# Kernel tuning notes

Hardware: AMD Instinct MI355X
Metric: run time of the kernel (lower is better)

Reference implementation:

```python
import jax, jax.numpy as jnp
import numpy as np

B, S, HID = 2, 2048, 2048
HQ, HKV, D = 32, 4, 128
EPS = 1e-6
SCALE = D ** -0.5


def _rms_norm(x, w):
    # per-head RMSNorm over last dim, computed in fp32 like the torch module
    xf = x.astype(jnp.float32)
    var = jnp.mean(xf * xf, axis=-1, keepdims=True)
    return (w * (xf * jax.lax.rsqrt(var + EPS))).astype(x.dtype)


def _rotate_half(x):
    x1, x2 = jnp.split(x, 2, axis=-1)
    return jnp.concatenate([-x2, x1], axis=-1)


def setup_inputs() -> dict:
    key = jax.random.key(0)
    ks = jax.random.split(key, 8)
    hidden_states = jax.random.normal(ks[0], (B, S, HID), dtype=jnp.float32)
    # RoPE tables (HF Qwen style, theta=1e6)
    inv_freq = 1.0 / (1e6 ** (np.arange(0, D, 2, dtype=np.float32) / D))
    t = np.arange(S, dtype=np.float32)
    freqs = np.outer(t, inv_freq)                      # [S, D/2]
    emb = np.concatenate([freqs, freqs], axis=-1)      # [S, D]
    cos = jnp.asarray(np.cos(emb))
    sin = jnp.asarray(np.sin(emb))
    sd = HID ** -0.5
    wq = jax.random.normal(ks[1], (HID, HQ * D), dtype=jnp.float32) * sd
    wk = jax.random.normal(ks[2], (HID, HKV * D), dtype=jnp.float32) * sd
    wv = jax.random.normal(ks[3], (HID, HKV * D), dtype=jnp.float32) * sd
    wo = jax.random.normal(ks[4], (HQ * D, HID), dtype=jnp.float32) * ((HQ * D) ** -0.5)
    q_norm_w = jnp.ones((D,), dtype=jnp.float32)
    k_norm_w = jnp.ones((D,), dtype=jnp.float32)
    return {"hidden_states": hidden_states, "cos": cos, "sin": sin,
            "wq": wq, "wk": wk, "wv": wv, "wo": wo,
            "q_norm_w": q_norm_w, "k_norm_w": k_norm_w}


def reference(hidden_states, cos, sin, wq, wk, wv, wo, q_norm_w, k_norm_w):
    b, s, _ = hidden_states.shape
    # QKV projection (no bias)
    q = (hidden_states @ wq).reshape(b, s, HQ, D)
    k = (hidden_states @ wk).reshape(b, s, HKV, D)
    v = (hidden_states @ wv).reshape(b, s, HKV, D)
    # per-head RMSNorm on q, k
    q = _rms_norm(q, q_norm_w)
    k = _rms_norm(k, k_norm_w)
    # RoPE: cos/sin [s, D] -> broadcast over batch and heads
    c = cos[None, :, None, :]
    sn = sin[None, :, None, :]
    q = q * c + _rotate_half(q) * sn
    k = k * c + _rotate_half(k) * sn
    # [b, h, s, d]
    q = q.transpose(0, 2, 1, 3)
    k = k.transpose(0, 2, 1, 3)
    v = v.transpose(0, 2, 1, 3)
    # GQA: repeat kv heads to match query heads
    groups = HQ // HKV
    k = jnp.repeat(k, groups, axis=1)
    v = jnp.repeat(v, groups, axis=1)
    # causal SDPA (prefill)
    scores = jnp.einsum('bhqd,bhkd->bhqk', q, k) * SCALE
    causal = jnp.tril(jnp.ones((s, s), dtype=bool))
    scores = jnp.where(causal[None, None], scores, jnp.finfo(scores.dtype).min)
    attn = jax.nn.softmax(scores, axis=-1)
    out = jnp.einsum('bhqk,bhkd->bhqd', attn, v)
    out = out.transpose(0, 2, 1, 3).reshape(b, s, HQ * D)
    return out @ wo
```

## Files before the change

### kernel.cpp

```cpp
#include <hip/hip_runtime.h>
#include <hip/hip_bf16.h>
#include <stdint.h>

typedef __bf16 bf16;
typedef __bf16 bf16x4 __attribute__((ext_vector_type(4)));
typedef __bf16 bf16x8 __attribute__((ext_vector_type(8)));
typedef float floatx4 __attribute__((ext_vector_type(4)));

#define MFMA16(a, b, c) __builtin_amdgcn_mfma_f32_16x16x32_bf16((a), (b), (c), 0, 0, 0)

static __device__ __forceinline__ void async_load16(const bf16* g, bf16* l) {
    __builtin_amdgcn_global_load_lds(
        (const __attribute__((address_space(1))) uint32_t*)(const void*)g,
        (__attribute__((address_space(3))) uint32_t*)(void*)l,
        16, 0, 0);
}

static __device__ __forceinline__ bf16x8 load8(const bf16* p) {
    return *(const bf16x8*)p;
}
static __device__ __forceinline__ bf16x8 load8(const float* p) {
    const float4 a = *(const float4*)p;
    const float4 b = *(const float4*)(p + 4);
    bf16x8 r;
    r[0] = (bf16)a.x; r[1] = (bf16)a.y; r[2] = (bf16)a.z; r[3] = (bf16)a.w;
    r[4] = (bf16)b.x; r[5] = (bf16)b.y; r[6] = (bf16)b.z; r[7] = (bf16)b.w;
    return r;
}

__global__ __launch_bounds__(256) void f2b(const float* __restrict__ in,
                                           bf16* __restrict__ out) {
    const size_t i = ((size_t)blockIdx.x * 256 + threadIdx.x) * 8;
    *(bf16x8*)&out[i] = load8(in + i);
}

__global__ __launch_bounds__(256) void transposeF2B(const float* __restrict__ in,
                                                    bf16* __restrict__ out,
                                                    int R, int C) {
    __shared__ float t[32][33];
    const int c0 = blockIdx.x * 32, r0 = blockIdx.y * 32;
    const int tx = threadIdx.x & 31, ty = threadIdx.x >> 5;
#pragma unroll
    for (int i = 0; i < 4; i++)
        t[ty + i * 8][tx] = in[(size_t)(r0 + ty + i * 8) * C + c0 + tx];
    __syncthreads();
#pragma unroll
    for (int i = 0; i < 4; i++)
        out[(size_t)(c0 + ty + i * 8) * R + r0 + tx] = (bf16)t[tx][ty + i * 8];
}

__global__ __launch_bounds__(256) void gemm_qkv(const bf16* __restrict__ A,
                                                const bf16* __restrict__ BT,
                                                bf16* __restrict__ Q,
                                                bf16* __restrict__ K2,
                                                bf16* __restrict__ Vt) {
    constexpr int K = 2048;
    __shared__ __attribute__((aligned(16))) bf16 As[2][128 * 64];
    __shared__ __attribute__((aligned(16))) bf16 Bs[2][128 * 64];
    const int tid = threadIdx.x;
    const int wave = tid >> 6, lane = tid & 63;
    const int quad = lane >> 4, l16 = lane & 15;
    const int m0 = blockIdx.y * 128, n0 = blockIdx.x * 128;
    const int wr = (wave >> 1) * 64, wc = (wave & 1) * 64;

    floatx4 acc[4][4] = {};

    const int wbase = wave * 32;
    const bf16* aSrc[4]; const bf16* bSrc[4];
#pragma unroll
    for (int j = 0; j < 4; j++) {
        const int r = wbase + 8 * j + (lane >> 3);
        aSrc[j] = A + (size_t)(m0 + r) * K + (((lane & 7) ^ (r & 7)) << 3);
        bSrc[j] = BT + (size_t)(n0 + r) * K + (((lane & 7) ^ (r & 7)) << 3);
    }

#define GSTAGE(buf, kk)                                                 \
    do {                                                                \
        bf16* aD_ = &As[buf][wbase * 64];                               \
        bf16* bD_ = &Bs[buf][wbase * 64];                               \
        _Pragma("unroll")                                               \
        for (int j_ = 0; j_ < 4; j_++) {                                \
            async_load16(aSrc[j_] + (kk), aD_ + j_ * 8 * 64);           \
            async_load16(bSrc[j_] + (kk), bD_ + j_ * 8 * 64);           \
        }                                                               \
    } while (0)

    constexpr int NKT = K / 64;
    GSTAGE(0, 0);
    int cur = 0;
    for (int kt = 0; kt < NKT; ++kt) {
        if (kt + 1 < NKT) {
            GSTAGE(cur ^ 1, (kt + 1) * 64);
            asm volatile("s_waitcnt vmcnt(8)" ::: "memory");
        } else {
            asm volatile("s_waitcnt vmcnt(0)" ::: "memory");
        }
        __builtin_amdgcn_s_barrier();
        __builtin_amdgcn_sched_barrier(0);

#pragma unroll
        for (int ks = 0; ks < 2; ks++) {
            const int slot = ((ks * 4 + quad) ^ (l16 & 7)) << 3;
            bf16x8 af[4], bfr[4];
#pragma unroll
            for (int i = 0; i < 4; i++)
                af[i] = *(const bf16x8*)&As[cur][(wr + i * 16 + l16) * 64 + slot];
#pragma unroll
            for (int j = 0; j < 4; j++)
                bfr[j] = *(const bf16x8*)&Bs[cur][(wc + j * 16 + l16) * 64 + slot];
#pragma unroll
            for (int i = 0; i < 4; i++)
#pragma unroll
                for (int j = 0; j < 4; j++)
                    acc[i][j] = MFMA16(af[i], bfr[j], acc[i][j]);
        }
        __builtin_amdgcn_s_barrier();
        cur ^= 1;
    }
#undef GSTAGE

    const int region = (n0 >= 4608) ? 2 : (n0 >= 4096 ? 1 : 0);
#pragma unroll
    for (int i = 0; i < 4; i++) {
#pragma unroll
        for (int j = 0; j < 4; j++) {
            const int row = m0 + wr + i * 16 + quad * 4;
            const int col = n0 + wc + j * 16 + l16;
            if (region == 0) {
#pragma unroll
                for (int r = 0; r < 4; r++)
                    Q[(size_t)(row + r) * 4096 + col] = (bf16)acc[i][j][r];
            } else if (region == 1) {
#pragma unroll
                for (int r = 0; r < 4; r++)
                    K2[(size_t)(row + r) * 512 + (col - 4096)] = (bf16)acc[i][j][r];
            } else {
                bf16x4 t;
#pragma unroll
                for (int r = 0; r < 4; r++) t[r] = (bf16)acc[i][j][r];
                *(bf16x4*)&Vt[(size_t)(col - 4608) * 4096 + row] = t;
            }
        }
    }
}

__global__ __launch_bounds__(256) void gemm_o(const bf16* __restrict__ A,
                                              const bf16* __restrict__ BT,
                                              float* __restrict__ C) {
    constexpr int K = 4096, N = 2048;
    __shared__ __attribute__((aligned(16))) bf16 As[2][128 * 64];
    __shared__ __attribute__((aligned(16))) bf16 Bs[2][128 * 64];
    const int tid = threadIdx.x;
    const int wave = tid >> 6, lane = tid & 63;
    const int quad = lane >> 4, l16 = lane & 15;
    const int m0 = blockIdx.y * 128, n0 = blockIdx.x * 128;
    const int wr = (wave >> 1) * 64, wc = (wave & 1) * 64;

    floatx4 acc[4][4] = {};

    const int wbase = wave * 32;
    const bf16* aSrc[4]; const bf16* bSrc[4];
#pragma unroll
    for (int j = 0; j < 4; j++) {
        const int r = wbase + 8 * j + (lane >> 3);
        aSrc[j] = A + (size_t)(m0 + r) * K + (((lane & 7) ^ (r & 7)) << 3);
        bSrc[j] = BT + (size_t)(n0 + r) * K + (((lane & 7) ^ (r & 7)) << 3);
    }

#define GSTAGE(buf, kk)                                                 \
    do {                                                                \
        bf16* aD_ = &As[buf][wbase * 64];                               \
        bf16* bD_ = &Bs[buf][wbase * 64];                               \
        _Pragma("unroll")                                               \
        for (int j_ = 0; j_ < 4; j_++) {                                \
            async_load16(aSrc[j_] + (kk), aD_ + j_ * 8 * 64);           \
            async_load16(bSrc[j_] + (kk), bD_ + j_ * 8 * 64);           \
        }                                                               \
    } while (0)

    constexpr int NKT = K / 64;
    GSTAGE(0, 0);
    int cur = 0;
    for (int kt = 0; kt < NKT; ++kt) {
        if (kt + 1 < NKT) {
            GSTAGE(cur ^ 1, (kt + 1) * 64);
            asm volatile("s_waitcnt vmcnt(8)" ::: "memory");
        } else {
            asm volatile("s_waitcnt vmcnt(0)" ::: "memory");
        }
        __builtin_amdgcn_s_barrier();
        __builtin_amdgcn_sched_barrier(0);

#pragma unroll
        for (int ks = 0; ks < 2; ks++) {
            const int slot = ((ks * 4 + quad) ^ (l16 & 7)) << 3;
            bf16x8 af[4], bfr[4];
#pragma unroll
            for (int i = 0; i < 4; i++)
                af[i] = *(const bf16x8*)&As[cur][(wr + i * 16 + l16) * 64 + slot];
#pragma unroll
            for (int j = 0; j < 4; j++)
                bfr[j] = *(const bf16x8*)&Bs[cur][(wc + j * 16 + l16) * 64 + slot];
#pragma unroll
            for (int i = 0; i < 4; i++)
#pragma unroll
                for (int j = 0; j < 4; j++)
                    acc[i][j] = MFMA16(af[i], bfr[j], acc[i][j]);
        }
        __builtin_amdgcn_s_barrier();
        cur ^= 1;
    }
#undef GSTAGE

#pragma unroll
    for (int i = 0; i < 4; i++) {
#pragma unroll
        for (int j = 0; j < 4; j++) {
            const int row = m0 + wr + i * 16 + quad * 4;
            const int col = n0 + wc + j * 16 + l16;
#pragma unroll
            for (int r = 0; r < 4; r++)
                C[(size_t)(row + r) * N + col] = acc[i][j][r];
        }
    }
}

__global__ __launch_bounds__(256) void rmsrope(bf16* __restrict__ x,
                                               const float* __restrict__ w,
                                               const float* __restrict__ cosb,
                                               const float* __restrict__ sinb,
                                               int nh, int S) {
    const int lane = threadIdx.x & 63;
    const int row = blockIdx.x * 4 + (threadIdx.x >> 6);
    const int s = (row / nh) % S;
    bf16* p = x + (size_t)row * 128;
    float x1 = (float)p[lane];
    float x2 = (float)p[lane + 64];
    float ssq = x1 * x1 + x2 * x2;
#pragma unroll
    for (int m = 1; m < 64; m <<= 1) ssq += __shfl_xor(ssq, m);
    const float r = rsqrtf(ssq * (1.0f / 128.0f) + 1e-6f);
    const float y1 = w[lane] * x1 * r;
    const float y2 = w[lane + 64] * x2 * r;
    const float c1 = cosb[s * 128 + lane];
    const float s1 = sinb[s * 128 + lane];
    const float c2 = cosb[s * 128 + lane + 64];
    const float s2 = sinb[s * 128 + lane + 64];
    p[lane] = (bf16)(y1 * c1 - y2 * s1);
    p[lane + 64] = (bf16)(y2 * c2 + y1 * s2);
}

__global__ __launch_bounds__(512, 4) void attn(bf16* QO,
                                               const bf16* __restrict__ Km,
                                               const bf16* __restrict__ Vt,
                                               int S) {
    __shared__ __attribute__((aligned(16))) bf16 Kl[2][64 * 128];
    __shared__ __attribute__((aligned(16))) bf16 Vl[2][128 * 64];
    __shared__ __attribute__((aligned(16))) bf16 Pl[8][16 * 40];

    const int tid = threadIdx.x, wave = tid >> 6, lane = tid & 63;
    const int quad = lane >> 4, l16 = lane & 15;
    const int h = blockIdx.y, b = blockIdx.z;
    const int kvh = h >> 3;
    const float scale = 0.08838834764831845f;

    const bf16* Kg = Km + (size_t)b * S * 512 + kvh * 128;
    const bf16* Vg = Vt + (size_t)kvh * 128 * 4096 + (size_t)b * S;

    const int krow0 = wave * 8 + (lane >> 4);
    const int krow1 = wave * 8 + 4 + (lane >> 4);
    const bf16* kSrc0 = Kg + (size_t)krow0 * 512 + (((lane & 15) ^ (krow0 & 7)) << 3);
    const bf16* kSrc1 = Kg + (size_t)krow1 * 512 + (((lane & 15) ^ (krow1 & 7)) << 3);
    const int vrow0 = wave * 16 + (lane >> 3);
    const int vrow1 = wave * 16 + 8 + (lane >> 3);
    const bf16* vSrc0 = Vg + (size_t)vrow0 * 4096 + (((lane & 7) ^ (vrow0 & 7)) << 3);
    const bf16* vSrc1 = Vg + (size_t)vrow1 * 4096 + (((lane & 7) ^ (vrow1 & 7)) << 3);

#define STAGE(buf, kk)                                                  \
    do {                                                                \
        bf16* kb_ = &Kl[buf][(wave * 8) * 128];                         \
        bf16* vb_ = &Vl[buf][(wave * 16) * 64];                         \
        async_load16(kSrc0 + (size_t)(kk) * 512, kb_);                  \
        async_load16(kSrc1 + (size_t)(kk) * 512, kb_ + 4 * 128);        \
        async_load16(vSrc0 + (kk), vb_);                                \
        async_load16(vSrc1 + (kk), vb_ + 8 * 64);                       \
    } while (0)

    bf16* pw = &Pl[wave][0];

#pragma unroll
    for (int half = 0; half < 2; half++) {
        const int qt = half ? (15 - blockIdx.x) : blockIdx.x;
        const int qb = qt * 128 + wave * 16;

        bf16x8 qf[4];
        {
            const bf16* qrow = QO + (size_t)(b * S + qb + l16) * 4096 + h * 128 + quad * 8;
#pragma unroll
            for (int c = 0; c < 4; c++) qf[c] = *(const bf16x8*)(qrow + c * 32);
        }

        floatx4 o_acc[8] = {};
        float l_i[4] = {0.f, 0.f, 0.f, 0.f};

        const int nt = 2 * (qt + 1);
        STAGE(0, 0);

        for (int kt = 0; kt < nt; ++kt) {
            const int k0 = kt * 64;
            const int cur = kt & 1;
            if (kt + 1 < nt) {
                STAGE(cur ^ 1, (kt + 1) * 64);
                asm volatile("s_waitcnt vmcnt(4)" ::: "memory");
            } else {
                asm volatile("s_waitcnt vmcnt(0)" ::: "memory");
            }
            __builtin_amdgcn_s_barrier();
            __builtin_amdgcn_sched_barrier(0);

            if (k0 <= qb + 15) {
                const bf16* kl = &Kl[cur][0];
                const bf16* vl = &Vl[cur][0];

                floatx4 sc[4] = {};
#pragma unroll
                for (int c = 0; c < 4; c++) {
                    const int slot = ((c * 4 + quad) ^ (l16 & 7)) << 3;
#pragma unroll
                    for (int m = 0; m < 4; m++) {
                        const bf16x8 kf = *(const bf16x8*)&kl[(l16 + 16 * m) * 128 + slot];
                        sc[m] = MFMA16(qf[c], kf, sc[m]);
                    }
                }

#pragma unroll
                for (int ks = 0; ks < 2; ks++) {
                    const int kb = k0 + ks * 32;
                    if (kb > qb + 15) continue;
                    const floatx4 s0 = sc[2 * ks], s1 = sc[2 * ks + 1];
                    if (kb + 31 > qb) {
#pragma unroll
                        for (int r = 0; r < 4; r++) {
                            const int qi = qb + quad * 4 + r;
                            const float p0 = (kb + l16 > qi) ? 0.f : __expf(s0[r] * scale);
                            const float p1 = (kb + 16 + l16 > qi) ? 0.f : __expf(s1[r] * scale);
                            l_i[r] += p0 + p1;
                            pw[(quad * 4 + r) * 40 + l16] = (bf16)p0;
                            pw[(quad * 4 + r) * 40 + l16 + 16] = (bf16)p1;
                        }
                    } else {
#pragma unroll
                        for (int r = 0; r < 4; r++) {
                            const float p0 = __expf(s0[r] * scale);
                            const float p1 = __expf(s1[r] * scale);
                            l_i[r] += p0 + p1;
                            pw[(quad * 4 + r) * 40 + l16] = (bf16)p0;
                            pw[(quad * 4 + r) * 40 + l16 + 16] = (bf16)p1;
                        }
                    }
                    const bf16x8 pa = *(const bf16x8*)&pw[l16 * 40 + quad * 8];
#pragma unroll
                    for (int c = 0; c < 8; c++) {
                        const int vps = ((ks * 4 + quad) ^ (l16 & 7)) << 3;
                        const bf16x8 vf = *(const bf16x8*)&vl[(c * 16 + l16) * 64 + vps];
                        o_acc[c] = MFMA16(pa, vf, o_acc[c]);
                    }
                }
            }
            __builtin_amdgcn_s_barrier();
        }

#pragma unroll
        for (int r = 0; r < 4; r++) {
            float l = l_i[r];
            l += __shfl_xor(l, 1);
            l += __shfl_xor(l, 2);
            l += __shfl_xor(l, 4);
            l += __shfl_xor(l, 8);
            const float inv = (l > 0.f) ? 1.0f / l : 0.f;
            const size_t orow = (size_t)(b * S + qb + quad * 4 + r) * 4096 + h * 128;
#pragma unroll
            for (int c = 0; c < 8; c++)
                QO[orow + c * 16 + l16] = (bf16)(o_acc[c][r] * inv);
        }
    }
#undef STAGE
}

template <typename TA, typename TB, typename TC>
__global__ __launch_bounds__(256) void gemm_bn(const TA* __restrict__ A,
                                               const TB* __restrict__ B,
                                               TC* __restrict__ C,
                                               int M, int N, int K) {
    __shared__ __attribute__((aligned(16))) bf16 As[128 * 32];
    __shared__ __attribute__((aligned(16))) bf16 Bs[128 * 32];
    const int tid = threadIdx.x;
    const int wave = tid >> 6, lane = tid & 63;
    const int quad = lane >> 4, l16 = lane & 15;
    const int m0 = blockIdx.y * 128, n0 = blockIdx.x * 128;
    const int wr = (wave >> 1) * 64, wc = (wave & 1) * 64;
    floatx4 acc[4][4] = {};
    const int r0 = tid >> 2;
    const int kc = (tid & 3) * 8;
    const TA* gA0 = A + (size_t)(m0 + r0) * K + kc;
    const TA* gA1 = A + (size_t)(m0 + 64 + r0) * K + kc;
    const int kr = tid & 31;
    const int nc8 = (tid >> 5) * 8;
    const TB* gB = B + (size_t)kr * N + n0 + nc8;
    for (int k0 = 0; k0 < K; k0 += 32) {
        const bf16x8 a0 = load8(gA0 + k0);
        const bf16x8 a1 = load8(gA1 + k0);
        const TB* gBk = gB + (size_t)k0 * N;
        const bf16x8 b0 = load8(gBk);
        const bf16x8 b1 = load8(gBk + 64);
        __syncthreads();
        *(bf16x8*)&As[r0 * 32 + kc] = a0;
        *(bf16x8*)&As[(64 + r0) * 32 + kc] = a1;
#pragma unroll
        for (int j = 0; j < 8; j++) {
            Bs[(nc8 + j) * 32 + kr] = b0[j];
            Bs[(nc8 + 64 + j) * 32 + kr] = b1[j];
        }
        __syncthreads();
        bf16x8 af[4], bfr[4];
#pragma unroll
        for (int i = 0; i < 4; i++)
            af[i] = *(const bf16x8*)&As[(wr + i * 16 + l16) * 32 + quad * 8];
#pragma unroll
        for (int j = 0; j < 4; j++)
            bfr[j] = *(const bf16x8*)&Bs[(wc + j * 16 + l16) * 32 + quad * 8];
#pragma unroll
        for (int i = 0; i < 4; i++)
#pragma unroll
            for (int j = 0; j < 4; j++)
                acc[i][j] = MFMA16(af[i], bfr[j], acc[i][j]);
    }
#pragma unroll
    for (int i = 0; i < 4; i++) {
#pragma unroll
        for (int j = 0; j < 4; j++) {
            const int row = m0 + wr + i * 16 + quad * 4;
            const int col = n0 + wc + j * 16 + l16;
#pragma unroll
            for (int r = 0; r < 4; r++)
                C[(size_t)(row + r) * N + col] = (TC)acc[i][j][r];
        }
    }
}

__global__ __launch_bounds__(256) void attn_fb(bf16* QO,
                                               const bf16* __restrict__ Km,
                                               const bf16* __restrict__ Vm,
                                               int S) {
    __shared__ __attribute__((aligned(16))) bf16 Kl[32 * 136];
    __shared__ __attribute__((aligned(16))) bf16 Vl[128 * 40];
    __shared__ __attribute__((aligned(16))) bf16 Pl[4][16 * 40];
    const int tid = threadIdx.x, wave = tid >> 6, lane = tid & 63;
    const int quad = lane >> 4, l16 = lane & 15;
    const int q0 = blockIdx.x * 64;
    const int h = blockIdx.y, b = blockIdx.z;
    const int kvh = h >> 3;
    const int q_base = q0 + wave * 16;
    const float scale = 0.08838834764831845f;
    bf16x8 qf[4];
    {
        const bf16* qrow = QO + (size_t)(b * S + q_base + l16) * 4096 + h * 128 + quad * 8;
#pragma unroll
        for (int c = 0; c < 4; c++) qf[c] = *(const bf16x8*)(qrow + c * 32);
    }
    floatx4 o_acc[8] = {};
    float l_i[4] = {0.f, 0.f, 0.f, 0.f};
    const int kend = q0 + 64;
    for (int k0 = 0; k0 < kend; k0 += 32) {
#pragma unroll
        for (int it = 0; it < 2; ++it) {
            const int cc = tid + it * 256;
            const int row = cc >> 4;
            const int off = (cc & 15) * 8;
            const size_t gidx = (size_t)(b * S + k0 + row) * 512 + kvh * 128 + off;
            const bf16x8 kv = *(const bf16x8*)&Km[gidx];
            const bf16x8 vv = *(const bf16x8*)&Vm[gidx];
            *(bf16x8*)&Kl[row * 136 + off] = kv;
#pragma unroll
            for (int j = 0; j < 8; j++) Vl[(off + j) * 40 + row] = vv[j];
        }
        __syncthreads();
        if (k0 <= q_base + 15) {
            floatx4 sc0 = {}, sc1 = {};
#pragma unroll
            for (int c = 0; c < 4; c++) {
                bf16x8 b0 = *(const bf16x8*)&Kl[l16 * 136 + c * 32 + quad * 8];
                bf16x8 b1 = *(const bf16x8*)&Kl[(l16 + 16) * 136 + c * 32 + quad * 8];
                sc0 = MFMA16(qf[c], b0, sc0);
                sc1 = MFMA16(qf[c], b1, sc1);
            }
            const bool edge = (k0 + 31 > q_base);
            bf16* pw = &Pl[wave][0];
#pragma unroll
            for (int r = 0; r < 4; r++) {
                const int qi = q_base + quad * 4 + r;
                const bool mk0 = edge && (k0 + l16 > qi);
                const bool mk1 = edge && (k0 + 16 + l16 > qi);
                const float p0 = mk0 ? 0.f : __expf(sc0[r] * scale);
                const float p1 = mk1 ? 0.f : __expf(sc1[r] * scale);
                l_i[r] += p0 + p1;
                pw[(quad * 4 + r) * 40 + l16] = (bf16)p0;
                pw[(quad * 4 + r) * 40 + l16 + 16] = (bf16)p1;
            }
            const bf16x8 pa = *(const bf16x8*)&pw[l16 * 40 + quad * 8];
#pragma unroll
            for (int c = 0; c < 8; c++) {
                const bf16x8 vf = *(const bf16x8*)&Vl[(c * 16 + l16) * 40 + quad * 8];
                o_acc[c] = MFMA16(pa, vf, o_acc[c]);
            }
        }
        __syncthreads();
    }
#pragma unroll
    for (int r = 0; r < 4; r++) {
        float l = l_i[r];
        l += __shfl_xor(l, 1);
        l += __shfl_xor(l, 2);
        l += __shfl_xor(l, 4);
        l += __shfl_xor(l, 8);
        const float inv = (l > 0.f) ? 1.0f / l : 0.f;
        const size_t orow = (size_t)(b * S + q_base + quad * 4 + r) * 4096 + h * 128;
#pragma unroll
        for (int c = 0; c < 8; c++)
            QO[orow + c * 16 + l16] = (bf16)(o_acc[c][r] * inv);
    }
}

extern "C" void kernel_launch(void* const* d_in, const int* in_sizes, int n_in,
                              void* d_out, int out_size, void* d_ws, size_t ws_size,
                              hipStream_t stream) {
    const float* hidden = (const float*)d_in[0];
    const float* cosb = (const float*)d_in[1];
    const float* sinb = (const float*)d_in[2];
    const float* wq = (const float*)d_in[3];
    const float* wk = (const float*)d_in[4];
    const float* wv = (const float*)d_in[5];
    const float* wo = (const float*)d_in[6];
    const float* qnw = (const float*)d_in[7];
    const float* knw = (const float*)d_in[8];
    float* out = (float*)d_out;

    constexpr int B = 2, S = 2048, HID = 2048, HQ = 32, HKV = 4, D = 128;
    constexpr int M = B * S;
    constexpr int NQ = HQ * D;
    constexpr int NKV = HKV * D;
    constexpr int NQKV = NQ + 2 * NKV;

    const size_t need = ((size_t)NQKV * HID + (size_t)HID * NQ +
                         (size_t)M * NQ + 2 * (size_t)M * NKV) * sizeof(bf16);

    if (ws_size >= need) {
        bf16* p = (bf16*)d_ws;
        bf16* wqkvT = p; p += (size_t)NQKV * HID;
        bf16* X = p;     p += (size_t)HID * NQ;
        bf16* Qb = p;    p += (size_t)M * NQ;
        bf16* Kb = p;    p += (size_t)M * NKV;
        bf16* Vt = p;    p += (size_t)NKV * M;

        transposeF2B<<<dim3(NQ / 32, HID / 32), 256, 0, stream>>>(wq, wqkvT, HID, NQ);
        transposeF2B<<<dim3(NKV / 32, HID / 32), 256, 0, stream>>>(wk, wqkvT + (size_t)NQ * HID, HID, NKV);
        transposeF2B<<<dim3(NKV / 32, HID / 32), 256, 0, stream>>>(wv, wqkvT + (size_t)(NQ + NKV) * HID, HID, NKV);

        f2b<<<dim3((M * HID) / (256 * 8)), 256, 0, stream>>>(hidden, X);

        gemm_qkv<<<dim3(NQKV / 128, M / 128), 256, 0, stream>>>(X, wqkvT, Qb, Kb, Vt);

        rmsrope<<<dim3(M * HQ / 4), 256, 0, stream>>>(Qb, qnw, cosb, sinb, HQ, S);
        rmsrope<<<dim3(M * HKV / 4), 256, 0, stream>>>(Kb, knw, cosb, sinb, HKV, S);

        attn<<<dim3(S / 256, HQ, B), 512, 0, stream>>>(Qb, Kb, Vt, S);

        transposeF2B<<<dim3(HID / 32, NQ / 32), 256, 0, stream>>>(wo, X, NQ, HID);
        gemm_o<<<dim3(HID / 128, M / 128), 256, 0, stream>>>(Qb, X, out);
    } else {
        bf16* p = (bf16*)d_ws;
        bf16* Qb = p;  p += (size_t)M * NQ;
        bf16* Kb = p;  p += (size_t)M * NKV;
        bf16* Vb = p;  p += (size_t)M * NKV;

        gemm_bn<float, float, bf16><<<dim3(NQ / 128, M / 128), 256, 0, stream>>>(hidden, wq, Qb, M, NQ, HID);
        gemm_bn<float, float, bf16><<<dim3(NKV / 128, M / 128), 256, 0, stream>>>(hidden, wk, Kb, M, NKV, HID);
        gemm_bn<float, float, bf16><<<dim3(NKV / 128, M / 128), 256, 0, stream>>>(hidden, wv, Vb, M, NKV, HID);
        rmsrope<<<dim3(M * HQ / 4), 256, 0, stream>>>(Qb, qnw, cosb, sinb, HQ, S);
        rmsrope<<<dim3(M * HKV / 4), 256, 0, stream>>>(Kb, knw, cosb, sinb, HKV, S);
        attn_fb<<<dim3(S / 64, HQ, B), 256, 0, stream>>>(Qb, Kb, Vb, S);
        gemm_bn<bf16, float, float><<<dim3(HID / 128, M / 128), 256, 0, stream>>>(Qb, wo, out, M, HID, NQ);
    }
}
```

Before: 474.4 us.

## Vectorize transpose and RMSNorm-RoPE, remap workgroups per XCD, fold softmax scale into Q

The transpose kernel now writes four bf16 values per thread instead of scalar stores. The RMSNorm+RoPE kernel uses 16 lanes per row with 8-element vector loads, and does rotate_half through a lane shuffle. GEMM and attention blocks are remapped so consecutive workgroups land on the same XCD, aiming to improve L2 reuse on the multi-die MI355X. The softmax scale is folded into Q during the norm pass, which removes a multiply per score in attention but rounds scaled Q to bf16 before the QK product.

```diff
diff --git a/kernel.cpp b/kernel.cpp
--- a/kernel.cpp
+++ b/kernel.cpp
@@ -44,9 +44,12 @@
     for (int i = 0; i < 4; i++)
         t[ty + i * 8][tx] = in[(size_t)(r0 + ty + i * 8) * C + c0 + tx];
     __syncthreads();
-#pragma unroll
-    for (int i = 0; i < 4; i++)
-        out[(size_t)(c0 + ty + i * 8) * R + r0 + tx] = (bf16)t[tx][ty + i * 8];
+    const int ow = threadIdx.x >> 3;
+    const int oc = (threadIdx.x & 7) * 4;
+    bf16x4 vo;
+#pragma unroll
+    for (int k = 0; k < 4; k++) vo[k] = (bf16)t[oc + k][ow];
+    *(bf16x4*)&out[(size_t)(c0 + ow) * R + r0 + oc] = vo;
 }
 
 __global__ __launch_bounds__(256) void gemm_qkv(const bf16* __restrict__ A,
@@ -60,7 +63,11 @@
     const int tid = threadIdx.x;
     const int wave = tid >> 6, lane = tid & 63;
     const int quad = lane >> 4, l16 = lane & 15;
-    const int m0 = blockIdx.y * 128, n0 = blockIdx.x * 128;
+    const int nwgx = gridDim.x;
+    const int nwg = nwgx * gridDim.y;
+    const int L = blockIdx.y * nwgx + blockIdx.x;
+    const int Lp = (L & 7) * (nwg >> 3) + (L >> 3);
+    const int m0 = (Lp / nwgx) * 128, n0 = (Lp % nwgx) * 128;
     const int wr = (wave >> 1) * 64, wc = (wave & 1) * 64;
 
     floatx4 acc[4][4] = {};
@@ -153,7 +160,11 @@
     const int tid = threadIdx.x;
     const int wave = tid >> 6, lane = tid & 63;
     const int quad = lane >> 4, l16 = lane & 15;
-    const int m0 = blockIdx.y * 128, n0 = blockIdx.x * 128;
+    const int nwgx = gridDim.x;
+    const int nwg = nwgx * gridDim.y;
+    const int L = blockIdx.y * nwgx + blockIdx.x;
+    const int Lp = (L & 7) * (nwg >> 3) + (L >> 3);
+    const int m0 = (Lp / nwgx) * 128, n0 = (Lp % nwgx) * 128;
     const int wr = (wave >> 1) * 64, wc = (wave & 1) * 64;
 
     floatx4 acc[4][4] = {};
@@ -229,25 +240,40 @@
                                                const float* __restrict__ w,
                                                const float* __restrict__ cosb,
                                                const float* __restrict__ sinb,
-                                               int nh, int S) {
-    const int lane = threadIdx.x & 63;
-    const int row = blockIdx.x * 4 + (threadIdx.x >> 6);
+                                               int nh, int S, float mul) {
+    const int l16 = threadIdx.x & 15;
+    const int row = blockIdx.x * 16 + (threadIdx.x >> 4);
     const int s = (row / nh) % S;
-    bf16* p = x + (size_t)row * 128;
-    float x1 = (float)p[lane];
-    float x2 = (float)p[lane + 64];
-    float ssq = x1 * x1 + x2 * x2;
-#pragma unroll
-    for (int m = 1; m < 64; m <<= 1) ssq += __shfl_xor(ssq, m);
-    const float r = rsqrtf(ssq * (1.0f / 128.0f) + 1e-6f);
-    const float y1 = w[lane] * x1 * r;
-    const float y2 = w[lane + 64] * x2 * r;
-    const float c1 = cosb[s * 128 + lane];
-    const float s1 = sinb[s * 128 + lane];
-    const float c2 = cosb[s * 128 + lane + 64];
-    const float s2 = sinb[s * 128 + lane + 64];
-    p[lane] = (bf16)(y1 * c1 - y2 * s1);
-    p[lane + 64] = (bf16)(y2 * c2 + y1 * s2);
+    const int e0 = l16 * 8;
+    bf16* p = x + (size_t)row * 128 + e0;
+    const bf16x8 v = *(const bf16x8*)p;
+    float xv[8], ssq = 0.f;
+#pragma unroll
+    for (int i = 0; i < 8; i++) { xv[i] = (float)v[i]; ssq += xv[i] * xv[i]; }
+#pragma unroll
+    for (int m = 1; m < 16; m <<= 1) ssq += __shfl_xor(ssq, m);
+    const float rm = rsqrtf(ssq * (1.0f / 128.0f) + 1e-6f) * mul;
+    const float4 w0 = *(const float4*)&w[e0];
+    const float4 w1 = *(const float4*)&w[e0 + 4];
+    float y[8];
+    y[0] = w0.x * xv[0] * rm; y[1] = w0.y * xv[1] * rm;
+    y[2] = w0.z * xv[2] * rm; y[3] = w0.w * xv[3] * rm;
+    y[4] = w1.x * xv[4] * rm; y[5] = w1.y * xv[5] * rm;
+    y[6] = w1.z * xv[6] * rm; y[7] = w1.w * xv[7] * rm;
+    const float sgn = (l16 < 8) ? -1.f : 1.f;
+    const float4 ca = *(const float4*)&cosb[s * 128 + e0];
+    const float4 cb2 = *(const float4*)&cosb[s * 128 + e0 + 4];
+    const float4 sa = *(const float4*)&sinb[s * 128 + e0];
+    const float4 sb2 = *(const float4*)&sinb[s * 128 + e0 + 4];
+    const float cc[8] = {ca.x, ca.y, ca.z, ca.w, cb2.x, cb2.y, cb2.z, cb2.w};
+    const float ss[8] = {sa.x, sa.y, sa.z, sa.w, sb2.x, sb2.y, sb2.z, sb2.w};
+    bf16x8 o;
+#pragma unroll
+    for (int i = 0; i < 8; i++) {
+        const float rot = sgn * __shfl_xor(y[i], 8);
+        o[i] = (bf16)(y[i] * cc[i] + rot * ss[i]);
+    }
+    *(bf16x8*)p = o;
 }
 
 __global__ __launch_bounds__(512, 4) void attn(bf16* QO,
@@ -260,9 +286,12 @@
 
     const int tid = threadIdx.x, wave = tid >> 6, lane = tid & 63;
     const int quad = lane >> 4, l16 = lane & 15;
-    const int h = blockIdx.y, b = blockIdx.z;
+    const int L = blockIdx.z * 256 + blockIdx.y * 8 + blockIdx.x;
+    const int Lp = ((L & 7) << 6) + (L >> 3);
+    const int bxs = Lp & 7;
+    const int h = (Lp >> 3) & 31;
+    const int b = Lp >> 8;
     const int kvh = h >> 3;
-    const float scale = 0.08838834764831845f;
 
     const bf16* Kg = Km + (size_t)b * S * 512 + kvh * 128;
     const bf16* Vg = Vt + (size_t)kvh * 128 * 4096 + (size_t)b * S;
@@ -290,7 +319,7 @@
 
 #pragma unroll
     for (int half = 0; half < 2; half++) {
-        const int qt = half ? (15 - blockIdx.x) : blockIdx.x;
+        const int qt = half ? (15 - bxs) : bxs;
         const int qb = qt * 128 + wave * 16;
 
         bf16x8 qf[4];
@@ -342,8 +371,8 @@
 #pragma unroll
                         for (int r = 0; r < 4; r++) {
                             const int qi = qb + quad * 4 + r;
-                            const float p0 = (kb + l16 > qi) ? 0.f : __expf(s0[r] * scale);
-                            const float p1 = (kb + 16 + l16 > qi) ? 0.f : __expf(s1[r] * scale);
+                            const float p0 = (kb + l16 > qi) ? 0.f : __expf(s0[r]);
+                            const float p1 = (kb + 16 + l16 > qi) ? 0.f : __expf(s1[r]);
                             l_i[r] += p0 + p1;
                             pw[(quad * 4 + r) * 40 + l16] = (bf16)p0;
                             pw[(quad * 4 + r) * 40 + l16 + 16] = (bf16)p1;
@@ -351,8 +380,8 @@
                     } else {
 #pragma unroll
                         for (int r = 0; r < 4; r++) {
-                            const float p0 = __expf(s0[r] * scale);
-                            const float p1 = __expf(s1[r] * scale);
+                            const float p0 = __expf(s0[r]);
+                            const float p1 = __expf(s1[r]);
                             l_i[r] += p0 + p1;
                             pw[(quad * 4 + r) * 40 + l16] = (bf16)p0;
                             pw[(quad * 4 + r) * 40 + l16 + 16] = (bf16)p1;
@@ -550,6 +579,7 @@
     constexpr int NQ = HQ * D;
     constexpr int NKV = HKV * D;
     constexpr int NQKV = NQ + 2 * NKV;
+    constexpr float SCALE = 0.08838834764831845f;
 
     const size_t need = ((size_t)NQKV * HID + (size_t)HID * NQ +
                          (size_t)M * NQ + 2 * (size_t)M * NKV) * sizeof(bf16);
@@ -570,8 +600,8 @@
 
         gemm_qkv<<<dim3(NQKV / 128, M / 128), 256, 0, stream>>>(X, wqkvT, Qb, Kb, Vt);
 
-        rmsrope<<<dim3(M * HQ / 4), 256, 0, stream>>>(Qb, qnw, cosb, sinb, HQ, S);
-        rmsrope<<<dim3(M * HKV / 4), 256, 0, stream>>>(Kb, knw, cosb, sinb, HKV, S);
+        rmsrope<<<dim3(M * HQ / 16), 256, 0, stream>>>(Qb, qnw, cosb, sinb, HQ, S, SCALE);
+        rmsrope<<<dim3(M * HKV / 16), 256, 0, stream>>>(Kb, knw, cosb, sinb, HKV, S, 1.0f);
 
         attn<<<dim3(S / 256, HQ, B), 512, 0, stream>>>(Qb, Kb, Vt, S);
 
@@ -586,8 +616,8 @@
         gemm_bn<float, float, bf16><<<dim3(NQ / 128, M / 128), 256, 0, stream>>>(hidden, wq, Qb, M, NQ, HID);
         gemm_bn<float, float, bf16><<<dim3(NKV / 128, M / 128), 256, 0, stream>>>(hidden, wk, Kb, M, NKV, HID);
         gemm_bn<float, float, bf16><<<dim3(NKV / 128, M / 128), 256, 0, stream>>>(hidden, wv, Vb, M, NKV, HID);
-        rmsrope<<<dim3(M * HQ / 4), 256, 0, stream>>>(Qb, qnw, cosb, sinb, HQ, S);
-        rmsrope<<<dim3(M * HKV / 4), 256, 0, stream>>>(Kb, knw, cosb, sinb, HKV, S);
+        rmsrope<<<dim3(M * HQ / 16), 256, 0, stream>>>(Qb, qnw, cosb, sinb, HQ, S, 1.0f);
+        rmsrope<<<dim3(M * HKV / 16), 256, 0, stream>>>(Kb, knw, cosb, sinb, HKV, S, 1.0f);
         attn_fb<<<dim3(S / 64, HQ, B), 256, 0, stream>>>(Qb, Kb, Vb, S);
         gemm_bn<bf16, float, float><<<dim3(HID / 128, M / 128), 256, 0, stream>>>(Qb, wo, out, M, HID, NQ);
     }
```

New measurement: 459.3 us. 3.2% less time.
